# Kernel optimization log

Hardware: AMD Instinct MI355X
Metric: run time of the kernel (lower is better)

## Reference

```python
import jax, jax.numpy as jnp
import numpy as np

N_FILTER = 64
IMAGE_SIZE = 64
CHANNELS = 3
N_CALLS = 16  # n_calls * 16 with n_calls=1
EPS = 1e-5


def _sobel_kernels(c):
    kx = jnp.array([[-1., 0., 1.], [-2., 0., 2.], [-1., 0., 1.]], jnp.float32) / 8.0
    ky = kx.T
    # depthwise OIHW kernels: (C, 1, 3, 3)
    return jnp.tile(kx[None, None], (c, 1, 1, 1)), jnp.tile(ky[None, None], (c, 1, 1, 1))


def _dwconv(x, k):
    return jax.lax.conv_general_dilated(
        x, k, window_strides=(1, 1), padding='SAME',
        feature_group_count=x.shape[1],
        dimension_numbers=('NCHW', 'OIHW', 'NCHW'))


def setup_inputs() -> dict:
    key = jax.random.key(0)
    k1, k2, k3 = jax.random.split(key, 3)
    B, L = 16, 512
    fin, fout = N_FILTER * 3, N_FILTER
    return {
        'lat': jax.random.normal(k1, (B, L), jnp.float32),
        'Wk': jax.random.normal(k2, (L, fin * fout), jnp.float32) * 0.02,
        'bk': jnp.zeros((fin * fout,), jnp.float32),
        'Wb': jax.random.normal(k3, (L, fout), jnp.float32) * 0.02,
        'bb': jnp.zeros((fout,), jnp.float32),
        'leak_factor': jnp.asarray(0.1, jnp.float32),
    }


def reference(lat, Wk, bk, Wb, bb, leak_factor):
    B = lat.shape[0]
    fin, fout = N_FILTER * 3, N_FILTER
    kx, ky = _sobel_kernels(N_FILTER)

    # seed: zeros with a 1.0 in channel 0 at the image center
    out0 = jnp.zeros((B, N_FILTER, IMAGE_SIZE, IMAGE_SIZE), jnp.float32)
    out0 = out0.at[:, 0, IMAGE_SIZE // 2, IMAGE_SIZE // 2].set(1.0)

    leak = jnp.clip(leak_factor, 0.001, 1000.0)

    # per-sample dynamic 1x1 conv weights/bias (constant across the loop)
    w = (lat @ Wk + bk).reshape(B, fout, fin)   # (B, fout, fin)
    b = (lat @ Wb + bb)                          # (B, fout)

    def step(out, _):
        # Sobel perception: [identity, grad_x, grad_y] -> (B, 3*nf, H, W)
        p = jnp.concatenate([out, _dwconv(out, kx), _dwconv(out, ky)], axis=1)
        # InstanceNorm2d (affine=False): normalize over H, W per sample/channel
        mu = p.mean(axis=(2, 3), keepdims=True)
        var = p.var(axis=(2, 3), keepdims=True)
        p = (p - mu) * jax.lax.rsqrt(var + EPS)
        # latent-conditioned dynamic 1x1 conv
        new = jnp.einsum('bchw,boc->bohw', p, w) + b[:, :, None, None]
        out = out + leak * new
        return out, out

    out, embs = jax.lax.scan(step, out0, None, length=N_CALLS)
    out_embs = jnp.concatenate([out0[None], embs], axis=0)  # (N_CALLS+1, B, nf, H, W)

    out_raw = out[:, :CHANNELS]
    return jnp.clip(out_raw, -1.0, 1.0), out_embs, out_raw
```

## Files before the change

### kernel.cpp

```cpp
#include <hip/hip_runtime.h>
#include <cstdint>
#include <cstddef>

#define NB 16
#define NC 64
#define HW 4096
#define SLICE ((size_t)(NB*NC*HW))
#define NSTEP 16

#define WS_WT    ((size_t)0)
#define WS_BV    ((size_t)196608)
#define WS_LATT  ((size_t)197632)
#define WS_SV    ((size_t)205824)
#define WS_SVMU  ((size_t)208896)

typedef _Float16 half8 __attribute__((ext_vector_type(8)));
typedef float f32x4 __attribute__((ext_vector_type(4)));

__global__ void k_latT(const float* __restrict__ lat, float* __restrict__ latT) {
  int t = threadIdx.x;
  for (int idx = t; idx < 16*512; idx += 256) {
    int b = idx >> 9, k = idx & 511;
    latT[k*16 + b] = lat[idx];
  }
}

__global__ __launch_bounds__(256) void k_w(const float* __restrict__ latT,
    const float* __restrict__ Wk, const float* __restrict__ bk,
    const float* __restrict__ Wb, const float* __restrict__ bb,
    float* __restrict__ wT, float* __restrict__ bvec) {
  int t = threadIdx.x;
  if (blockIdx.x < 48) {
    int j = blockIdx.x*256 + t;
    float acc[16];
#pragma unroll
    for (int b = 0; b < 16; b++) acc[b] = 0.f;
#pragma unroll 4
    for (int k = 0; k < 512; k++) {
      float wv = Wk[(size_t)k*12288 + j];
      const float* lt = (const float*)__builtin_assume_aligned(latT + k*16, 64);
#pragma unroll
      for (int b = 0; b < 16; b++) acc[b] = fmaf(lt[b], wv, acc[b]);
    }
    int o = j / 192, cf = j % 192;
    int g = cf >> 6, c = cf & 63;
    float bkj = bk[j];
#pragma unroll
    for (int b = 0; b < 16; b++)
      wT[(((size_t)(b*3 + g))*64 + o)*64 + c] = acc[b] + bkj;
  } else if (t < 64) {
    int j = t;
    float acc[16];
#pragma unroll
    for (int b = 0; b < 16; b++) acc[b] = 0.f;
    for (int k = 0; k < 512; k++) {
      float wv = Wb[k*64 + j];
      const float* lt = (const float*)__builtin_assume_aligned(latT + k*16, 64);
#pragma unroll
      for (int b = 0; b < 16; b++) acc[b] = fmaf(lt[b], wv, acc[b]);
    }
    float bbj = bb[j];
#pragma unroll
    for (int b = 0; b < 16; b++) bvec[b*64 + j] = acc[b] + bbj;
  }
}

__global__ void k_init(float* __restrict__ e0) {
  int idx4 = (blockIdx.x*256 + threadIdx.x) * 4;
  float4 v = make_float4(0.f, 0.f, 0.f, 0.f);
  if ((idx4 & 262143) == 2080) v.x = 1.0f;
  *(float4*)(e0 + idx4) = v;
}

__global__ __launch_bounds__(256) void k_stats(const float* __restrict__ st,
    float* __restrict__ svb, float* __restrict__ svmub) {
  int c = blockIdx.x, b = blockIdx.y, t = threadIdx.x;
  __shared__ float red[4][6];
  const float* base = st + (size_t)(b*NC + c) * HW;
  int w = t & 63, wv = t >> 6, h0 = wv * 16;
  float s0=0,q0=0,s1=0,q1=0,s2=0,q2=0;

  float d_prev=0.f, s_prev=0.f, d_cur, s_cur, v_cur;
#define MKDS(X, D, S)                                  \
  {                                                    \
    float xl = __shfl((X), (w + 63) & 63);             \
    float xr = __shfl((X), (w + 1) & 63);              \
    if (w == 0)  xl = 0.f;                             \
    if (w == 63) xr = 0.f;                             \
    (D) = xr - xl; (S) = xl + 2.f*(X) + xr;            \
  }
  if (h0 > 0) {
    float x = base[(h0-1)*64 + w];
    MKDS(x, d_prev, s_prev)
  }
  {
    float x = base[h0*64 + w];
    MKDS(x, d_cur, s_cur)
    v_cur = x;
  }
#pragma unroll
  for (int k = 0; k < 16; k++) {
    int hn = h0 + k + 1;
    float d_nxt=0.f, s_nxt=0.f, v_nxt=0.f;
    if (hn < 64) {
      float x = base[hn*64 + w];
      MKDS(x, d_nxt, s_nxt)
      v_nxt = x;
    }
    float gx = (d_prev + 2.f*d_cur + d_nxt) * 0.125f;
    float gy = (s_nxt - s_prev) * 0.125f;
    s0 += v_cur; q0 = fmaf(v_cur, v_cur, q0);
    s1 += gx;    q1 = fmaf(gx, gx, q1);
    s2 += gy;    q2 = fmaf(gy, gy, q2);
    d_prev = d_cur; s_prev = s_cur;
    d_cur = d_nxt; s_cur = s_nxt; v_cur = v_nxt;
  }
#undef MKDS
#pragma unroll
  for (int off = 32; off >= 1; off >>= 1) {
    s0 += __shfl_xor(s0, off); q0 += __shfl_xor(q0, off);
    s1 += __shfl_xor(s1, off); q1 += __shfl_xor(q1, off);
    s2 += __shfl_xor(s2, off); q2 += __shfl_xor(q2, off);
  }
  int lane = t & 63;
  if (lane == 0) {
    red[wv][0]=s0; red[wv][1]=q0; red[wv][2]=s1;
    red[wv][3]=q1; red[wv][4]=s2; red[wv][5]=q2;
  }
  __syncthreads();
  if (t == 0) {
    float r[6];
#pragma unroll
    for (int u = 0; u < 6; u++) r[u] = red[0][u]+red[1][u]+red[2][u]+red[3][u];
#pragma unroll
    for (int g = 0; g < 3; g++) {
      float mu  = r[2*g] * (1.f/HW);
      float var = fmaxf(r[2*g+1]*(1.f/HW) - mu*mu, 0.f);
      float sv  = 1.f / sqrtf(var + 1e-5f);
      svb  [b*192 + g*64 + c] = sv;
      svmub[b*192 + g*64 + c] = sv * mu;
    }
  }
}

struct SB2 {
  alignas(16) _Float16 Bhi[6144];
  alignas(16) _Float16 Blo[6144];
  alignas(16) _Float16 Whi[2][6144];
  alignas(16) _Float16 Wlo[2][6144];
  float svL[192], svmuL[192], biasL[192], bvecL[64];
};

__global__ __launch_bounds__(256, 2) void k_fused(const float* __restrict__ st,
    float* __restrict__ stn, const float* __restrict__ wT,
    const float* __restrict__ bvec, const float* __restrict__ svb,
    const float* __restrict__ svmub, const float* __restrict__ leakp,
    float* __restrict__ out0, float* __restrict__ out2, int last) {
  __shared__ SB2 sh;
  int bid = blockIdx.x, t = threadIdx.x;
  int b = bid >> 5;
  int r0 = (bid & 7) * 8 + ((bid >> 3) & 3) * 2;
  int lane = t & 63, wt = t >> 6;
  const float* stb = st + (size_t)b*NC*HW;
  float leak = fminf(fmaxf(leakp[0], 0.001f), 1000.f);

  if (t < 192) { sh.svL[t] = svb[b*192 + t]; sh.svmuL[t] = svmub[b*192 + t]; }
  if (t < 64) sh.bvecL[t] = bvec[b*64 + t];
  __syncthreads();

  if (t < 192) {
    int g = t >> 6, o = t & 63;
    float biasacc = 0.f;
#pragma unroll
    for (int kc = 0; kc < 2; kc++) {
      const float* wrow = wT + (((size_t)(b*3 + g))*64 + o)*64 + kc*32;
#pragma unroll
      for (int s = 0; s < 4; s++) {
        float4 va = *(const float4*)(wrow + s*8);
        float4 vb4 = *(const float4*)(wrow + s*8 + 4);
        float wv[8] = {va.x,va.y,va.z,va.w,vb4.x,vb4.y,vb4.z,vb4.w};
        half8 hv, lv;
#pragma unroll
        for (int jj = 0; jj < 8; jj++) {
          int cg = g*64 + kc*32 + s*8 + jj;
          float scaled = wv[jj] * sh.svL[cg];
          biasacc = fmaf(wv[jj], sh.svmuL[cg], biasacc);
          _Float16 h = (_Float16)scaled;
          hv[jj] = h;
          lv[jj] = (_Float16)(scaled - (float)h);
        }
        int swz = (s ^ (o & 3) ^ ((o >> 2) & 3)) & 3;
        int sidx = (g*64 + o)*32 + (swz << 3);
        *(half8*)(&sh.Whi[kc][sidx]) = hv;
        *(half8*)(&sh.Wlo[kc][sidx]) = lv;
      }
    }
    sh.biasL[t] = biasacc;
  }

#define LOADW(KC, R, XW)                                                 \
  _Pragma("unroll")                                                      \
  for (int i = 0; i < 3; i++) {                                          \
    int u = t + i*256;                                                   \
    int c8 = u / 192, pxu = u % 192;                                     \
    int rho = pxu >> 6, ww = pxu & 63;                                   \
    int row = (R) - 1 + rho;                                             \
    bool ok = (row >= 0) && (row < 64);                                  \
    int rowc = ok ? row : 0;                                             \
    const float* gp = stb + (size_t)((KC)*32 + c8*8)*HW + rowc*64 + ww;  \
    _Pragma("unroll")                                                    \
    for (int ii = 0; ii < 8; ii++) {                                     \
      float val = gp[(size_t)ii*HW];                                     \
      XW[i][ii] = ok ? val : 0.f;                                        \
    }                                                                    \
  }

#define PACKW(XW)                                                        \
  _Pragma("unroll")                                                      \
  for (int i = 0; i < 3; i++) {                                          \
    int u = t + i*256;                                                   \
    int c8 = u / 192, pxu = u % 192;                                     \
    half8 hv, lv;                                                        \
    _Pragma("unroll")                                                    \
    for (int ii = 0; ii < 8; ii++) {                                     \
      float x = XW[i][ii];                                               \
      _Float16 h = (_Float16)x;                                          \
      hv[ii] = h;                                                        \
      lv[ii] = (_Float16)(x - (float)h);                                 \
    }                                                                    \
    int di = (c8*192 + (pxu ^ c8)) * 8;                                  \
    *(half8*)(sh.Bhi + di) = hv;                                         \
    *(half8*)(sh.Blo + di) = lv;                                         \
  }

#define MFMAS(KC)                                                        \
  {                                                                      \
    half8 ahi[3], alo[3];                                                \
    int oa = wt*16 + (lane & 15);                                        \
    int c4 = lane >> 4;                                                  \
    int slotx = (c4 ^ (oa & 3) ^ ((oa >> 2) & 3)) & 3;                   \
    _Pragma("unroll")                                                    \
    for (int g = 0; g < 3; g++) {                                        \
      int sidx = (g*64 + oa)*32 + (slotx << 3);                          \
      ahi[g] = *(const half8*)(&sh.Whi[KC][sidx]);                       \
      alo[g] = *(const half8*)(&sh.Wlo[KC][sidx]);                       \
    }                                                                    \
    _Pragma("unroll")                                                    \
    for (int n = 0; n < 12; n++) {                                       \
      int px = n*16 + (lane & 15);                                       \
      int bidx = (c4*192 + (px ^ c4))*8;                                 \
      half8 bh = *(const half8*)(sh.Bhi + bidx);                         \
      half8 bl = *(const half8*)(sh.Blo + bidx);                         \
      accB[n] = __builtin_amdgcn_mfma_f32_16x16x32_f16(ahi[1], bh, accB[n], 0,0,0); \
      accB[n] = __builtin_amdgcn_mfma_f32_16x16x32_f16(ahi[1], bl, accB[n], 0,0,0); \
      accB[n] = __builtin_amdgcn_mfma_f32_16x16x32_f16(alo[1], bh, accB[n], 0,0,0); \
      accC[n] = __builtin_amdgcn_mfma_f32_16x16x32_f16(ahi[2], bh, accC[n], 0,0,0); \
      accC[n] = __builtin_amdgcn_mfma_f32_16x16x32_f16(ahi[2], bl, accC[n], 0,0,0); \
      accC[n] = __builtin_amdgcn_mfma_f32_16x16x32_f16(alo[2], bh, accC[n], 0,0,0); \
      if (n >= 4 && n < 8) {                                             \
        accA[n-4] = __builtin_amdgcn_mfma_f32_16x16x32_f16(ahi[0], bh, accA[n-4], 0,0,0); \
        accA[n-4] = __builtin_amdgcn_mfma_f32_16x16x32_f16(ahi[0], bl, accA[n-4], 0,0,0); \
        accA[n-4] = __builtin_amdgcn_mfma_f32_16x16x32_f16(alo[0], bh, accA[n-4], 0,0,0); \
      }                                                                  \
    }                                                                    \
  }

#pragma unroll
  for (int rr = 0; rr < 2; rr++) {
    int r = r0 + rr;
    f32x4 accA[4] = {}; f32x4 accB[12] = {}; f32x4 accC[12] = {};
    float xw0[3][8], xw1[3][8];

    LOADW(0, r, xw0)
    __syncthreads();
    PACKW(xw0)
    __syncthreads();
    LOADW(1, r, xw1)
    MFMAS(0)
    __syncthreads();
    PACKW(xw1)
    __syncthreads();
    MFMAS(1)

#pragma unroll
    for (int j = 0; j < 4; j++) {
      int o = wt*16 + ((lane >> 4) << 2) + j;
      float Sx[4], Sy[4];
#pragma unroll
      for (int nc = 0; nc < 4; nc++) {
        Sx[nc] = accB[nc][j] + 2.f*accB[4+nc][j] + accB[8+nc][j];
        Sy[nc] = accC[8+nc][j] - accC[nc][j];
      }
      float bt = sh.bvecL[o] - sh.biasL[o] - sh.biasL[64+o] - sh.biasL[128+o];
#pragma unroll
      for (int nc = 0; nc < 4; nc++) {
        int nm = (nc > 0) ? nc-1 : 0;
        int np = (nc < 3) ? nc+1 : 3;
        float xl1 = __shfl(Sx[nc], (lane - 1) & 63);
        float xl2 = (nc > 0) ? __shfl(Sx[nm], (lane + 15) & 63) : 0.f;
        float xL  = (lane & 15) ? xl1 : xl2;
        float xr1 = __shfl(Sx[nc], (lane + 1) & 63);
        float xr2 = (nc < 3) ? __shfl(Sx[np], (lane - 15) & 63) : 0.f;
        float xR  = ((lane & 15) == 15) ? xr2 : xr1;
        float yl1 = __shfl(Sy[nc], (lane - 1) & 63);
        float yl2 = (nc > 0) ? __shfl(Sy[nm], (lane + 15) & 63) : 0.f;
        float yL  = (lane & 15) ? yl1 : yl2;
        float yr1 = __shfl(Sy[nc], (lane + 1) & 63);
        float yr2 = (nc < 3) ? __shfl(Sy[np], (lane - 15) & 63) : 0.f;
        float yR  = ((lane & 15) == 15) ? yr2 : yr1;
        float gx = (xR - xL) * 0.125f;
        float gy = (yL + 2.f*Sy[nc] + yR) * 0.125f;
        float nw = accA[nc][j] + gx + gy + bt;
        int wpx = nc*16 + (lane & 15);
        size_t gi = (size_t)(b*NC + o)*HW + (size_t)r*64 + wpx;
        float nv = st[gi] + leak * nw;
        stn[gi] = nv;
        if (last && o < 3) {
          size_t oi = (size_t)(b*3 + o)*HW + (size_t)r*64 + wpx;
          out2[oi] = nv;
          out0[oi] = fminf(fmaxf(nv, -1.f), 1.f);
        }
      }
    }
  }
#undef LOADW
#undef PACKW
#undef MFMAS
}

extern "C" void kernel_launch(void* const* d_in, const int* in_sizes, int n_in,
                              void* d_out, int out_size, void* d_ws, size_t ws_size,
                              hipStream_t stream) {
  const float* lat   = (const float*)d_in[0];
  const float* Wk    = (const float*)d_in[1];
  const float* bk    = (const float*)d_in[2];
  const float* Wb    = (const float*)d_in[3];
  const float* bb    = (const float*)d_in[4];
  const float* leakp = (const float*)d_in[5];
  float* out = (float*)d_out;
  float* ws  = (float*)d_ws;
  float* wT    = ws + WS_WT;
  float* bvec  = ws + WS_BV;
  float* latT  = ws + WS_LATT;
  float* svbuf = ws + WS_SV;
  float* svmub = ws + WS_SVMU;
  float* out0 = out;
  float* embs = out + 196608;
  float* out2 = out + 196608 + 17*SLICE;

  hipLaunchKernelGGL(k_latT, dim3(1),    dim3(256), 0, stream, lat, latT);
  hipLaunchKernelGGL(k_w,    dim3(49),   dim3(256), 0, stream, latT, Wk, bk, Wb, bb, wT, bvec);
  hipLaunchKernelGGL(k_init, dim3(4096), dim3(256), 0, stream, embs);
  for (int tstep = 0; tstep < NSTEP; tstep++) {
    const float* stc = embs + (size_t)tstep*SLICE;
    float*       stn = embs + (size_t)(tstep+1)*SLICE;
    hipLaunchKernelGGL(k_stats, dim3(64,16), dim3(256), 0, stream, stc, svbuf, svmub);
    hipLaunchKernelGGL(k_fused, dim3(512), dim3(256), 0, stream,
                       stc, stn, wT, bvec, svbuf, svmub, leakp,
                       out0, out2, (int)(tstep == NSTEP-1));
  }
}
```

Baseline: 599.8 us.

## Fuse stats and step kernels via cooperative launch with grid barrier

Merges the per-step statistics kernel and the fused MFMA update kernel into one cooperative kernel of 256 blocks of 512 threads. Stats are computed first, then a software grid barrier on global atomics separates them from the 1x1-conv update. Each block now runs two 256-thread groups with separate B buffers in shared memory. The lat transpose kernel is removed and k_w reads lat directly. This cuts kernel launches and inter-kernel gaps, but adds barrier spin cost, uses more LDS per block, and halves the grid, which may reduce occupancy.

```diff
diff --git a/kernel.cpp b/kernel.cpp
--- a/kernel.cpp
+++ b/kernel.cpp
@@ -7,25 +7,18 @@
 #define HW 4096
 #define SLICE ((size_t)(NB*NC*HW))
 #define NSTEP 16
+#define GRIDB 256
 
 #define WS_WT    ((size_t)0)
 #define WS_BV    ((size_t)196608)
-#define WS_LATT  ((size_t)197632)
 #define WS_SV    ((size_t)205824)
 #define WS_SVMU  ((size_t)208896)
+#define WS_BAR   ((size_t)211968)
 
 typedef _Float16 half8 __attribute__((ext_vector_type(8)));
 typedef float f32x4 __attribute__((ext_vector_type(4)));
 
-__global__ void k_latT(const float* __restrict__ lat, float* __restrict__ latT) {
-  int t = threadIdx.x;
-  for (int idx = t; idx < 16*512; idx += 256) {
-    int b = idx >> 9, k = idx & 511;
-    latT[k*16 + b] = lat[idx];
-  }
-}
-
-__global__ __launch_bounds__(256) void k_w(const float* __restrict__ latT,
+__global__ __launch_bounds__(256) void k_w(const float* __restrict__ lat,
     const float* __restrict__ Wk, const float* __restrict__ bk,
     const float* __restrict__ Wb, const float* __restrict__ bb,
     float* __restrict__ wT, float* __restrict__ bvec) {
@@ -38,9 +31,8 @@
 #pragma unroll 4
     for (int k = 0; k < 512; k++) {
       float wv = Wk[(size_t)k*12288 + j];
-      const float* lt = (const float*)__builtin_assume_aligned(latT + k*16, 64);
-#pragma unroll
-      for (int b = 0; b < 16; b++) acc[b] = fmaf(lt[b], wv, acc[b]);
+#pragma unroll
+      for (int b = 0; b < 16; b++) acc[b] = fmaf(lat[b*512 + k], wv, acc[b]);
     }
     int o = j / 192, cf = j % 192;
     int g = cf >> 6, c = cf & 63;
@@ -55,9 +47,8 @@
     for (int b = 0; b < 16; b++) acc[b] = 0.f;
     for (int k = 0; k < 512; k++) {
       float wv = Wb[k*64 + j];
-      const float* lt = (const float*)__builtin_assume_aligned(latT + k*16, 64);
-#pragma unroll
-      for (int b = 0; b < 16; b++) acc[b] = fmaf(lt[b], wv, acc[b]);
+#pragma unroll
+      for (int b = 0; b < 16; b++) acc[b] = fmaf(lat[b*512 + k], wv, acc[b]);
     }
     float bbj = bb[j];
 #pragma unroll
@@ -65,21 +56,48 @@
   }
 }
 
-__global__ void k_init(float* __restrict__ e0) {
+__global__ void k_init(float* __restrict__ e0, unsigned* __restrict__ bar) {
+  if (blockIdx.x == 0 && threadIdx.x == 0) { bar[0] = 0u; bar[1] = 0u; }
   int idx4 = (blockIdx.x*256 + threadIdx.x) * 4;
   float4 v = make_float4(0.f, 0.f, 0.f, 0.f);
   if ((idx4 & 262143) == 2080) v.x = 1.0f;
   *(float4*)(e0 + idx4) = v;
 }
 
-__global__ __launch_bounds__(256) void k_stats(const float* __restrict__ st,
-    float* __restrict__ svb, float* __restrict__ svmub) {
-  int c = blockIdx.x, b = blockIdx.y, t = threadIdx.x;
-  __shared__ float red[4][6];
+__device__ __forceinline__ void gridbar(unsigned* bar) {
+  __syncthreads();
+  if (threadIdx.x == 0) {
+    __threadfence();
+    unsigned g = __hip_atomic_load(&bar[1], __ATOMIC_RELAXED, __HIP_MEMORY_SCOPE_AGENT);
+    unsigned v = __hip_atomic_fetch_add(&bar[0], 1u, __ATOMIC_ACQ_REL, __HIP_MEMORY_SCOPE_AGENT);
+    if (v == (unsigned)(GRIDB - 1)) {
+      __hip_atomic_store(&bar[0], 0u, __ATOMIC_RELAXED, __HIP_MEMORY_SCOPE_AGENT);
+      __hip_atomic_fetch_add(&bar[1], 1u, __ATOMIC_RELEASE, __HIP_MEMORY_SCOPE_AGENT);
+    } else {
+      while (__hip_atomic_load(&bar[1], __ATOMIC_ACQUIRE, __HIP_MEMORY_SCOPE_AGENT) == g)
+        __builtin_amdgcn_s_sleep(1);
+    }
+    __threadfence();
+  }
+  __syncthreads();
+}
+
+struct SBC {
+  alignas(16) _Float16 Bhi[2][6144];
+  alignas(16) _Float16 Blo[2][6144];
+  alignas(16) _Float16 Whi[2][6144];
+  alignas(16) _Float16 Wlo[2][6144];
+  float svL[192], svmuL[192], biasL[192], bvecL[64];
+  float red[2][4][6];
+};
+
+__device__ void statsOne(SBC& sh, int grp, int t8, int b, int c,
+                         const float* __restrict__ st,
+                         float* __restrict__ svb, float* __restrict__ svmub) {
+  __syncthreads();
   const float* base = st + (size_t)(b*NC + c) * HW;
-  int w = t & 63, wv = t >> 6, h0 = wv * 16;
+  int w = t8 & 63, wv = t8 >> 6, h0 = wv * 16;
   float s0=0,q0=0,s1=0,q1=0,s2=0,q2=0;
-
   float d_prev=0.f, s_prev=0.f, d_cur, s_cur, v_cur;
 #define MKDS(X, D, S)                                  \
   {                                                    \
@@ -122,16 +140,17 @@
     s1 += __shfl_xor(s1, off); q1 += __shfl_xor(q1, off);
     s2 += __shfl_xor(s2, off); q2 += __shfl_xor(q2, off);
   }
-  int lane = t & 63;
+  int lane = t8 & 63;
   if (lane == 0) {
-    red[wv][0]=s0; red[wv][1]=q0; red[wv][2]=s1;
-    red[wv][3]=q1; red[wv][4]=s2; red[wv][5]=q2;
-  }
-  __syncthreads();
-  if (t == 0) {
+    sh.red[grp][wv][0]=s0; sh.red[grp][wv][1]=q0; sh.red[grp][wv][2]=s1;
+    sh.red[grp][wv][3]=q1; sh.red[grp][wv][4]=s2; sh.red[grp][wv][5]=q2;
+  }
+  __syncthreads();
+  if (t8 == 0) {
     float r[6];
 #pragma unroll
-    for (int u = 0; u < 6; u++) r[u] = red[0][u]+red[1][u]+red[2][u]+red[3][u];
+    for (int u = 0; u < 6; u++)
+      r[u] = sh.red[grp][0][u]+sh.red[grp][1][u]+sh.red[grp][2][u]+sh.red[grp][3][u];
 #pragma unroll
     for (int g = 0; g < 3; g++) {
       float mu  = r[2*g] * (1.f/HW);
@@ -143,24 +162,24 @@
   }
 }
 
-struct SB2 {
-  alignas(16) _Float16 Bhi[6144];
-  alignas(16) _Float16 Blo[6144];
-  alignas(16) _Float16 Whi[2][6144];
-  alignas(16) _Float16 Wlo[2][6144];
-  float svL[192], svmuL[192], biasL[192], bvecL[64];
-};
-
-__global__ __launch_bounds__(256, 2) void k_fused(const float* __restrict__ st,
+__global__ __launch_bounds__(512, 2) void k_step(const float* __restrict__ st,
     float* __restrict__ stn, const float* __restrict__ wT,
-    const float* __restrict__ bvec, const float* __restrict__ svb,
-    const float* __restrict__ svmub, const float* __restrict__ leakp,
-    float* __restrict__ out0, float* __restrict__ out2, int last) {
-  __shared__ SB2 sh;
+    const float* __restrict__ bvec, float* __restrict__ svb,
+    float* __restrict__ svmub, const float* __restrict__ leakp,
+    float* __restrict__ out0, float* __restrict__ out2,
+    unsigned* __restrict__ bar, int last) {
+  __shared__ SBC sh;
   int bid = blockIdx.x, t = threadIdx.x;
-  int b = bid >> 5;
-  int r0 = (bid & 7) * 8 + ((bid >> 3) & 3) * 2;
-  int lane = t & 63, wt = t >> 6;
+  int grp = t >> 8, t8 = t & 255;
+  int b = bid >> 4;
+
+  int c0 = (bid & 15) * 4 + grp * 2;
+  statsOne(sh, grp, t8, b, c0,     st, svb, svmub);
+  statsOne(sh, grp, t8, b, c0 + 1, st, svb, svmub);
+  gridbar(bar);
+
+  int xcd = bid & 7, ii = (bid >> 3) & 1;
+  int lane = t8 & 63, wt = t8 >> 6;
   const float* stb = st + (size_t)b*NC*HW;
   float leak = fminf(fmaxf(leakp[0], 0.001f), 1000.f);
 
@@ -201,7 +220,7 @@
 #define LOADW(KC, R, XW)                                                 \
   _Pragma("unroll")                                                      \
   for (int i = 0; i < 3; i++) {                                          \
-    int u = t + i*256;                                                   \
+    int u = t8 + i*256;                                                  \
     int c8 = u / 192, pxu = u % 192;                                     \
     int rho = pxu >> 6, ww = pxu & 63;                                   \
     int row = (R) - 1 + rho;                                             \
@@ -209,28 +228,28 @@
     int rowc = ok ? row : 0;                                             \
     const float* gp = stb + (size_t)((KC)*32 + c8*8)*HW + rowc*64 + ww;  \
     _Pragma("unroll")                                                    \
-    for (int ii = 0; ii < 8; ii++) {                                     \
-      float val = gp[(size_t)ii*HW];                                     \
-      XW[i][ii] = ok ? val : 0.f;                                        \
+    for (int ii2 = 0; ii2 < 8; ii2++) {                                  \
+      float val = gp[(size_t)ii2*HW];                                    \
+      XW[i][ii2] = ok ? val : 0.f;                                       \
     }                                                                    \
   }
 
 #define PACKW(XW)                                                        \
   _Pragma("unroll")                                                      \
   for (int i = 0; i < 3; i++) {                                          \
-    int u = t + i*256;                                                   \
+    int u = t8 + i*256;                                                  \
     int c8 = u / 192, pxu = u % 192;                                     \
     half8 hv, lv;                                                        \
     _Pragma("unroll")                                                    \
-    for (int ii = 0; ii < 8; ii++) {                                     \
-      float x = XW[i][ii];                                               \
+    for (int ii2 = 0; ii2 < 8; ii2++) {                                  \
+      float x = XW[i][ii2];                                              \
       _Float16 h = (_Float16)x;                                          \
-      hv[ii] = h;                                                        \
-      lv[ii] = (_Float16)(x - (float)h);                                 \
+      hv[ii2] = h;                                                       \
+      lv[ii2] = (_Float16)(x - (float)h);                                \
     }                                                                    \
     int di = (c8*192 + (pxu ^ c8)) * 8;                                  \
-    *(half8*)(sh.Bhi + di) = hv;                                         \
-    *(half8*)(sh.Blo + di) = lv;                                         \
+    *(half8*)(&sh.Bhi[grp][di]) = hv;                                    \
+    *(half8*)(&sh.Blo[grp][di]) = lv;                                    \
   }
 
 #define MFMAS(KC)                                                        \
@@ -249,8 +268,8 @@
     for (int n = 0; n < 12; n++) {                                       \
       int px = n*16 + (lane & 15);                                       \
       int bidx = (c4*192 + (px ^ c4))*8;                                 \
-      half8 bh = *(const half8*)(sh.Bhi + bidx);                         \
-      half8 bl = *(const half8*)(sh.Blo + bidx);                         \
+      half8 bh = *(const half8*)(&sh.Bhi[grp][bidx]);                    \
+      half8 bl = *(const half8*)(&sh.Blo[grp][bidx]);                    \
       accB[n] = __builtin_amdgcn_mfma_f32_16x16x32_f16(ahi[1], bh, accB[n], 0,0,0); \
       accB[n] = __builtin_amdgcn_mfma_f32_16x16x32_f16(ahi[1], bl, accB[n], 0,0,0); \
       accB[n] = __builtin_amdgcn_mfma_f32_16x16x32_f16(alo[1], bh, accB[n], 0,0,0); \
@@ -267,7 +286,7 @@
 
 #pragma unroll
   for (int rr = 0; rr < 2; rr++) {
-    int r = r0 + rr;
+    int r = xcd*8 + ii*4 + grp*2 + rr;
     f32x4 accA[4] = {}; f32x4 accB[12] = {}; f32x4 accC[12] = {};
     float xw0[3][8], xw1[3][8];
 
@@ -341,22 +360,23 @@
   float* ws  = (float*)d_ws;
   float* wT    = ws + WS_WT;
   float* bvec  = ws + WS_BV;
-  float* latT  = ws + WS_LATT;
   float* svbuf = ws + WS_SV;
   float* svmub = ws + WS_SVMU;
+  unsigned* bar = (unsigned*)(ws + WS_BAR);
   float* out0 = out;
   float* embs = out + 196608;
   float* out2 = out + 196608 + 17*SLICE;
 
-  hipLaunchKernelGGL(k_latT, dim3(1),    dim3(256), 0, stream, lat, latT);
-  hipLaunchKernelGGL(k_w,    dim3(49),   dim3(256), 0, stream, latT, Wk, bk, Wb, bb, wT, bvec);
-  hipLaunchKernelGGL(k_init, dim3(4096), dim3(256), 0, stream, embs);
+  hipLaunchKernelGGL(k_w,    dim3(49),   dim3(256), 0, stream, lat, Wk, bk, Wb, bb, wT, bvec);
+  hipLaunchKernelGGL(k_init, dim3(4096), dim3(256), 0, stream, embs, bar);
   for (int tstep = 0; tstep < NSTEP; tstep++) {
     const float* stc = embs + (size_t)tstep*SLICE;
     float*       stn = embs + (size_t)(tstep+1)*SLICE;
-    hipLaunchKernelGGL(k_stats, dim3(64,16), dim3(256), 0, stream, stc, svbuf, svmub);
-    hipLaunchKernelGGL(k_fused, dim3(512), dim3(256), 0, stream,
-                       stc, stn, wT, bvec, svbuf, svmub, leakp,
-                       out0, out2, (int)(tstep == NSTEP-1));
-  }
-}
+    int last = (tstep == NSTEP-1);
+    void* args[] = { (void*)&stc, (void*)&stn, (void*)&wT, (void*)&bvec,
+                     (void*)&svbuf, (void*)&svmub, (void*)&leakp,
+                     (void*)&out0, (void*)&out2, (void*)&bar, (void*)&last };
+    hipLaunchCooperativeKernel((void*)k_step, dim3(GRIDB), dim3(512),
+                               args, 0, stream);
+  }
+}
```

Result: slower. 1.307 ms (+117.9%).

## Fuse next-step instance-norm statistics into step kernel via halo recompute and atomics

Applied to the files above, without the earlier changes.

Removes the per-step statistics kernel. Each step block now recomputes one halo row above and below its two output rows, keeps the new state in registers, and computes the Sobel gradients and sum/sum-of-squares for the next step, adding them to a rotating triple-buffered stats array with atomics. The consumer turns the sums into mean and inverse std, and the latT transpose kernel is dropped so lat is read directly. This saves one full state read and one launch per step, but doubles the GEMM and MFMA work per block for the halo rows and adds atomic contention.

```diff
diff --git a/kernel.cpp b/kernel.cpp
--- a/kernel.cpp
+++ b/kernel.cpp
@@ -10,22 +10,12 @@
 
 #define WS_WT    ((size_t)0)
 #define WS_BV    ((size_t)196608)
-#define WS_LATT  ((size_t)197632)
-#define WS_SV    ((size_t)205824)
-#define WS_SVMU  ((size_t)208896)
+#define WS_STATS ((size_t)197632)
 
 typedef _Float16 half8 __attribute__((ext_vector_type(8)));
 typedef float f32x4 __attribute__((ext_vector_type(4)));
 
-__global__ void k_latT(const float* __restrict__ lat, float* __restrict__ latT) {
-  int t = threadIdx.x;
-  for (int idx = t; idx < 16*512; idx += 256) {
-    int b = idx >> 9, k = idx & 511;
-    latT[k*16 + b] = lat[idx];
-  }
-}
-
-__global__ __launch_bounds__(256) void k_w(const float* __restrict__ latT,
+__global__ __launch_bounds__(256) void k_w(const float* __restrict__ lat,
     const float* __restrict__ Wk, const float* __restrict__ bk,
     const float* __restrict__ Wb, const float* __restrict__ bb,
     float* __restrict__ wT, float* __restrict__ bvec) {
@@ -38,9 +28,8 @@
 #pragma unroll 4
     for (int k = 0; k < 512; k++) {
       float wv = Wk[(size_t)k*12288 + j];
-      const float* lt = (const float*)__builtin_assume_aligned(latT + k*16, 64);
-#pragma unroll
-      for (int b = 0; b < 16; b++) acc[b] = fmaf(lt[b], wv, acc[b]);
+#pragma unroll
+      for (int b = 0; b < 16; b++) acc[b] = fmaf(lat[b*512 + k], wv, acc[b]);
     }
     int o = j / 192, cf = j % 192;
     int g = cf >> 6, c = cf & 63;
@@ -55,9 +44,8 @@
     for (int b = 0; b < 16; b++) acc[b] = 0.f;
     for (int k = 0; k < 512; k++) {
       float wv = Wb[k*64 + j];
-      const float* lt = (const float*)__builtin_assume_aligned(latT + k*16, 64);
-#pragma unroll
-      for (int b = 0; b < 16; b++) acc[b] = fmaf(lt[b], wv, acc[b]);
+#pragma unroll
+      for (int b = 0; b < 16; b++) acc[b] = fmaf(lat[b*512 + k], wv, acc[b]);
     }
     float bbj = bb[j];
 #pragma unroll
@@ -65,21 +53,25 @@
   }
 }
 
-__global__ void k_init(float* __restrict__ e0) {
-  int idx4 = (blockIdx.x*256 + threadIdx.x) * 4;
+__global__ void k_init(float* __restrict__ e0, float* __restrict__ buf1) {
+  int bid = blockIdx.x, t = threadIdx.x;
+  if (bid == 0) {
+#pragma unroll
+    for (int i = 0; i < 24; i++) buf1[i*256 + t] = 0.f;
+  }
+  int idx4 = (bid*256 + t) * 4;
   float4 v = make_float4(0.f, 0.f, 0.f, 0.f);
   if ((idx4 & 262143) == 2080) v.x = 1.0f;
   *(float4*)(e0 + idx4) = v;
 }
 
-__global__ __launch_bounds__(256) void k_stats(const float* __restrict__ st,
-    float* __restrict__ svb, float* __restrict__ svmub) {
+__global__ __launch_bounds__(256) void k_stats0(const float* __restrict__ st,
+    float* __restrict__ sbuf) {
   int c = blockIdx.x, b = blockIdx.y, t = threadIdx.x;
   __shared__ float red[4][6];
   const float* base = st + (size_t)(b*NC + c) * HW;
   int w = t & 63, wv = t >> 6, h0 = wv * 16;
   float s0=0,q0=0,s1=0,q1=0,s2=0,q2=0;
-
   float d_prev=0.f, s_prev=0.f, d_cur, s_cur, v_cur;
 #define MKDS(X, D, S)                                  \
   {                                                    \
@@ -134,11 +126,9 @@
     for (int u = 0; u < 6; u++) r[u] = red[0][u]+red[1][u]+red[2][u]+red[3][u];
 #pragma unroll
     for (int g = 0; g < 3; g++) {
-      float mu  = r[2*g] * (1.f/HW);
-      float var = fmaxf(r[2*g+1]*(1.f/HW) - mu*mu, 0.f);
-      float sv  = 1.f / sqrtf(var + 1e-5f);
-      svb  [b*192 + g*64 + c] = sv;
-      svmub[b*192 + g*64 + c] = sv * mu;
+      size_t base2 = ((size_t)(b*3 + g)*64 + c)*2;
+      sbuf[base2]     = r[2*g];
+      sbuf[base2 + 1] = r[2*g + 1];
     }
   }
 }
@@ -151,10 +141,11 @@
   float svL[192], svmuL[192], biasL[192], bvecL[64];
 };
 
-__global__ __launch_bounds__(256, 2) void k_fused(const float* __restrict__ st,
+__global__ __launch_bounds__(256, 2) void k_step(const float* __restrict__ st,
     float* __restrict__ stn, const float* __restrict__ wT,
-    const float* __restrict__ bvec, const float* __restrict__ svb,
-    const float* __restrict__ svmub, const float* __restrict__ leakp,
+    const float* __restrict__ bvec, const float* __restrict__ statsR,
+    float* __restrict__ statsW, float* __restrict__ statsZ,
+    const float* __restrict__ leakp,
     float* __restrict__ out0, float* __restrict__ out2, int last) {
   __shared__ SB2 sh;
   int bid = blockIdx.x, t = threadIdx.x;
@@ -164,7 +155,16 @@
   const float* stb = st + (size_t)b*NC*HW;
   float leak = fminf(fmaxf(leakp[0], 0.001f), 1000.f);
 
-  if (t < 192) { sh.svL[t] = svb[b*192 + t]; sh.svmuL[t] = svmub[b*192 + t]; }
+  if (t < 12) statsZ[bid*12 + t] = 0.f;
+
+  if (t < 192) {
+    float s = statsR[(b*192 + t)*2];
+    float q = statsR[(b*192 + t)*2 + 1];
+    float mu = s * (1.f/HW);
+    float var = fmaxf(q*(1.f/HW) - mu*mu, 0.f);
+    float sv = 1.f / sqrtf(var + 1e-5f);
+    sh.svL[t] = sv; sh.svmuL[t] = sv * mu;
+  }
   if (t < 64) sh.bvecL[t] = bvec[b*64 + t];
   __syncthreads();
 
@@ -209,9 +209,9 @@
     int rowc = ok ? row : 0;                                             \
     const float* gp = stb + (size_t)((KC)*32 + c8*8)*HW + rowc*64 + ww;  \
     _Pragma("unroll")                                                    \
-    for (int ii = 0; ii < 8; ii++) {                                     \
-      float val = gp[(size_t)ii*HW];                                     \
-      XW[i][ii] = ok ? val : 0.f;                                        \
+    for (int e8 = 0; e8 < 8; e8++) {                                     \
+      float val = gp[(size_t)e8*HW];                                     \
+      XW[i][e8] = ok ? val : 0.f;                                        \
     }                                                                    \
   }
 
@@ -222,11 +222,11 @@
     int c8 = u / 192, pxu = u % 192;                                     \
     half8 hv, lv;                                                        \
     _Pragma("unroll")                                                    \
-    for (int ii = 0; ii < 8; ii++) {                                     \
-      float x = XW[i][ii];                                               \
+    for (int e8 = 0; e8 < 8; e8++) {                                     \
+      float x = XW[i][e8];                                               \
       _Float16 h = (_Float16)x;                                          \
-      hv[ii] = h;                                                        \
-      lv[ii] = (_Float16)(x - (float)h);                                 \
+      hv[e8] = h;                                                        \
+      lv[e8] = (_Float16)(x - (float)h);                                 \
     }                                                                    \
     int di = (c8*192 + (pxu ^ c8)) * 8;                                  \
     *(half8*)(sh.Bhi + di) = hv;                                         \
@@ -265,67 +265,131 @@
     }                                                                    \
   }
 
-#pragma unroll
-  for (int rr = 0; rr < 2; rr++) {
-    int r = r0 + rr;
-    f32x4 accA[4] = {}; f32x4 accB[12] = {}; f32x4 accC[12] = {};
-    float xw0[3][8], xw1[3][8];
-
-    LOADW(0, r, xw0)
-    __syncthreads();
-    PACKW(xw0)
-    __syncthreads();
-    LOADW(1, r, xw1)
-    MFMAS(0)
-    __syncthreads();
-    PACKW(xw1)
-    __syncthreads();
-    MFMAS(1)
-
-#pragma unroll
-    for (int j = 0; j < 4; j++) {
-      int o = wt*16 + ((lane >> 4) << 2) + j;
-      float Sx[4], Sy[4];
-#pragma unroll
-      for (int nc = 0; nc < 4; nc++) {
-        Sx[nc] = accB[nc][j] + 2.f*accB[4+nc][j] + accB[8+nc][j];
-        Sy[nc] = accC[8+nc][j] - accC[nc][j];
-      }
-      float bt = sh.bvecL[o] - sh.biasL[o] - sh.biasL[64+o] - sh.biasL[128+o];
-#pragma unroll
-      for (int nc = 0; nc < 4; nc++) {
-        int nm = (nc > 0) ? nc-1 : 0;
-        int np = (nc < 3) ? nc+1 : 3;
-        float xl1 = __shfl(Sx[nc], (lane - 1) & 63);
-        float xl2 = (nc > 0) ? __shfl(Sx[nm], (lane + 15) & 63) : 0.f;
-        float xL  = (lane & 15) ? xl1 : xl2;
-        float xr1 = __shfl(Sx[nc], (lane + 1) & 63);
-        float xr2 = (nc < 3) ? __shfl(Sx[np], (lane - 15) & 63) : 0.f;
-        float xR  = ((lane & 15) == 15) ? xr2 : xr1;
-        float yl1 = __shfl(Sy[nc], (lane - 1) & 63);
-        float yl2 = (nc > 0) ? __shfl(Sy[nm], (lane + 15) & 63) : 0.f;
-        float yL  = (lane & 15) ? yl1 : yl2;
-        float yr1 = __shfl(Sy[nc], (lane + 1) & 63);
-        float yr2 = (nc < 3) ? __shfl(Sy[np], (lane - 15) & 63) : 0.f;
-        float yR  = ((lane & 15) == 15) ? yr2 : yr1;
-        float gx = (xR - xL) * 0.125f;
-        float gy = (yL + 2.f*Sy[nc] + yR) * 0.125f;
-        float nw = accA[nc][j] + gx + gy + bt;
-        int wpx = nc*16 + (lane & 15);
-        size_t gi = (size_t)(b*NC + o)*HW + (size_t)r*64 + wpx;
-        float nv = st[gi] + leak * nw;
-        stn[gi] = nv;
-        if (last && o < 3) {
-          size_t oi = (size_t)(b*3 + o)*HW + (size_t)r*64 + wpx;
-          out2[oi] = nv;
-          out0[oi] = fminf(fmaxf(nv, -1.f), 1.f);
+  float nv4[4][16];
+
+#pragma unroll
+  for (int rr = 0; rr < 4; rr++) {
+    int r = r0 - 1 + rr;
+    if (r >= 0 && r < 64) {
+      f32x4 accA[4] = {}; f32x4 accB[12] = {}; f32x4 accC[12] = {};
+      float xw0[3][8], xw1[3][8];
+
+      LOADW(0, r, xw0)
+      __syncthreads();
+      PACKW(xw0)
+      __syncthreads();
+      LOADW(1, r, xw1)
+      MFMAS(0)
+      __syncthreads();
+      PACKW(xw1)
+      __syncthreads();
+      MFMAS(1)
+
+#pragma unroll
+      for (int j = 0; j < 4; j++) {
+        int o = wt*16 + ((lane >> 4) << 2) + j;
+        float Sx[4], Sy[4];
+#pragma unroll
+        for (int nc = 0; nc < 4; nc++) {
+          Sx[nc] = accB[nc][j] + 2.f*accB[4+nc][j] + accB[8+nc][j];
+          Sy[nc] = accC[8+nc][j] - accC[nc][j];
         }
-      }
+        float bt = sh.bvecL[o] - sh.biasL[o] - sh.biasL[64+o] - sh.biasL[128+o];
+#pragma unroll
+        for (int nc = 0; nc < 4; nc++) {
+          int nm = (nc > 0) ? nc-1 : 0;
+          int np = (nc < 3) ? nc+1 : 3;
+          float xl1 = __shfl(Sx[nc], (lane - 1) & 63);
+          float xl2 = (nc > 0) ? __shfl(Sx[nm], (lane + 15) & 63) : 0.f;
+          float xL  = (lane & 15) ? xl1 : xl2;
+          float xr1 = __shfl(Sx[nc], (lane + 1) & 63);
+          float xr2 = (nc < 3) ? __shfl(Sx[np], (lane - 15) & 63) : 0.f;
+          float xR  = ((lane & 15) == 15) ? xr2 : xr1;
+          float yl1 = __shfl(Sy[nc], (lane - 1) & 63);
+          float yl2 = (nc > 0) ? __shfl(Sy[nm], (lane + 15) & 63) : 0.f;
+          float yL  = (lane & 15) ? yl1 : yl2;
+          float yr1 = __shfl(Sy[nc], (lane + 1) & 63);
+          float yr2 = (nc < 3) ? __shfl(Sy[np], (lane - 15) & 63) : 0.f;
+          float yR  = ((lane & 15) == 15) ? yr2 : yr1;
+          float gx = (xR - xL) * 0.125f;
+          float gy = (yL + 2.f*Sy[nc] + yR) * 0.125f;
+          float nw = accA[nc][j] + gx + gy + bt;
+          int wpx = nc*16 + (lane & 15);
+          size_t gi = (size_t)(b*NC + o)*HW + (size_t)r*64 + wpx;
+          float nv = st[gi] + leak * nw;
+          nv4[rr][j*4 + nc] = nv;
+          if (rr == 1 || rr == 2) {
+            stn[gi] = nv;
+            if (last && o < 3) {
+              size_t oi = (size_t)(b*3 + o)*HW + (size_t)r*64 + wpx;
+              out2[oi] = nv;
+              out0[oi] = fminf(fmaxf(nv, -1.f), 1.f);
+            }
+          }
+        }
+      }
+    } else {
+#pragma unroll
+      for (int u = 0; u < 16; u++) nv4[rr][u] = 0.f;
     }
   }
 #undef LOADW
 #undef PACKW
 #undef MFMAS
+
+  if (!last) {
+#pragma unroll
+    for (int j = 0; j < 4; j++) {
+      float dxv[4][4], sxv[4][4];
+#pragma unroll
+      for (int rw = 0; rw < 4; rw++) {
+        float vv[4];
+#pragma unroll
+        for (int nc = 0; nc < 4; nc++) vv[nc] = nv4[rw][j*4 + nc];
+#pragma unroll
+        for (int nc = 0; nc < 4; nc++) {
+          int nm = (nc > 0) ? nc-1 : 0;
+          int np = (nc < 3) ? nc+1 : 3;
+          float xl1 = __shfl(vv[nc], (lane - 1) & 63);
+          float xl2 = (nc > 0) ? __shfl(vv[nm], (lane + 15) & 63) : 0.f;
+          float xL  = (lane & 15) ? xl1 : xl2;
+          float xr1 = __shfl(vv[nc], (lane + 1) & 63);
+          float xr2 = (nc < 3) ? __shfl(vv[np], (lane - 15) & 63) : 0.f;
+          float xR  = ((lane & 15) == 15) ? xr2 : xr1;
+          dxv[rw][nc] = xR - xL;
+          sxv[rw][nc] = xL + 2.f*vv[nc] + xR;
+        }
+      }
+      float s0=0,q0=0,s1=0,q1=0,s2=0,q2=0;
+#pragma unroll
+      for (int rr = 1; rr <= 2; rr++) {
+#pragma unroll
+        for (int nc = 0; nc < 4; nc++) {
+          float v = nv4[rr][j*4 + nc];
+          s0 += v; q0 = fmaf(v, v, q0);
+          float gx = (dxv[rr-1][nc] + 2.f*dxv[rr][nc] + dxv[rr+1][nc]) * 0.125f;
+          float gy = (sxv[rr+1][nc] - sxv[rr-1][nc]) * 0.125f;
+          s1 += gx; q1 = fmaf(gx, gx, q1);
+          s2 += gy; q2 = fmaf(gy, gy, q2);
+        }
+      }
+#pragma unroll
+      for (int m = 1; m <= 8; m <<= 1) {
+        s0 += __shfl_xor(s0, m); q0 += __shfl_xor(q0, m);
+        s1 += __shfl_xor(s1, m); q1 += __shfl_xor(q1, m);
+        s2 += __shfl_xor(s2, m); q2 += __shfl_xor(q2, m);
+      }
+      if ((lane & 15) == 0) {
+        int o = wt*16 + ((lane >> 4) << 2) + j;
+        atomicAdd(&statsW[((size_t)(b*3 + 0)*64 + o)*2    ], s0);
+        atomicAdd(&statsW[((size_t)(b*3 + 0)*64 + o)*2 + 1], q0);
+        atomicAdd(&statsW[((size_t)(b*3 + 1)*64 + o)*2    ], s1);
+        atomicAdd(&statsW[((size_t)(b*3 + 1)*64 + o)*2 + 1], q1);
+        atomicAdd(&statsW[((size_t)(b*3 + 2)*64 + o)*2    ], s2);
+        atomicAdd(&statsW[((size_t)(b*3 + 2)*64 + o)*2 + 1], q2);
+      }
+    }
+  }
 }
 
 extern "C" void kernel_launch(void* const* d_in, const int* in_sizes, int n_in,
@@ -341,22 +405,23 @@
   float* ws  = (float*)d_ws;
   float* wT    = ws + WS_WT;
   float* bvec  = ws + WS_BV;
-  float* latT  = ws + WS_LATT;
-  float* svbuf = ws + WS_SV;
-  float* svmub = ws + WS_SVMU;
+  float* sb0   = ws + WS_STATS;
+  float* sb1   = ws + WS_STATS + 6144;
+  float* sb2   = ws + WS_STATS + 12288;
+  float* sbuf[3] = { sb0, sb1, sb2 };
   float* out0 = out;
   float* embs = out + 196608;
   float* out2 = out + 196608 + 17*SLICE;
 
-  hipLaunchKernelGGL(k_latT, dim3(1),    dim3(256), 0, stream, lat, latT);
-  hipLaunchKernelGGL(k_w,    dim3(49),   dim3(256), 0, stream, latT, Wk, bk, Wb, bb, wT, bvec);
-  hipLaunchKernelGGL(k_init, dim3(4096), dim3(256), 0, stream, embs);
+  hipLaunchKernelGGL(k_w,      dim3(49),     dim3(256), 0, stream, lat, Wk, bk, Wb, bb, wT, bvec);
+  hipLaunchKernelGGL(k_init,   dim3(4096),   dim3(256), 0, stream, embs, sb1);
+  hipLaunchKernelGGL(k_stats0, dim3(64,16),  dim3(256), 0, stream, embs, sb0);
   for (int tstep = 0; tstep < NSTEP; tstep++) {
     const float* stc = embs + (size_t)tstep*SLICE;
     float*       stn = embs + (size_t)(tstep+1)*SLICE;
-    hipLaunchKernelGGL(k_stats, dim3(64,16), dim3(256), 0, stream, stc, svbuf, svmub);
-    hipLaunchKernelGGL(k_fused, dim3(512), dim3(256), 0, stream,
-                       stc, stn, wT, bvec, svbuf, svmub, leakp,
-                       out0, out2, (int)(tstep == NSTEP-1));
+    hipLaunchKernelGGL(k_step, dim3(512), dim3(256), 0, stream,
+                       stc, stn, wT, bvec,
+                       sbuf[tstep % 3], sbuf[(tstep+1) % 3], sbuf[(tstep+2) % 3],
+                       leakp, out0, out2, (int)(tstep == NSTEP-1));
   }
 }
```

Result: slower. 910.3 us (+51.8%).
